# Optimization experiments

Hardware: AMD Instinct MI355X
Metric: run time of the kernel (lower is better)

## Reference

```python
import jax, jax.numpy as jnp
import numpy as np

B, S, NH, D_IN = 64, 512, 4, 256   # batch, seq_len, rnn n_head, input_dim
H = 256                            # hidden_dim == attention activation_dim
AH = 256                           # attention_hidden_dim (attn out_dim)
OUT = 3                            # output_dim (sentiment classes)


def setup_inputs() -> dict:
    key = jax.random.key(0)
    ks = jax.random.split(key, 9)
    def p(k, shape, scale=0.05):
        return jax.random.normal(k, shape, dtype=jnp.float32) * scale
    return dict(
        x=jax.random.normal(ks[0], (B, S, NH, D_IN), dtype=jnp.float32),
        Wk=p(ks[1], (D_IN, H)), bk=jnp.zeros((H,), jnp.float32),
        Wq=p(ks[2], (H, H)),    bq=jnp.zeros((H,), jnp.float32),
        w_mlp=p(ks[3], (2 * H,)),
        Wproj=p(ks[4], (H, AH)), bproj=jnp.zeros((AH,), jnp.float32),
        W1=p(ks[5], (D_IN + AH, H)), b1=jnp.zeros((H,), jnp.float32),
        W2=p(ks[6], (H, H)),    b2=jnp.zeros((H,), jnp.float32),
        Wo=p(ks[7], (NH * H, OUT)), bo=jnp.zeros((OUT,), jnp.float32),
    )


def _cell(x_t, hidden, params):
    Wk, bk, Wq, bq, w_mlp, Wproj, bproj, W1, b1, W2, b2, Wo, bo = params
    kx = x_t @ Wk + bk           # [B, NH, H]  keys from step input
    qx = hidden @ Wq + bq        # [B, NH, H]  queries from hidden state
    w1, w2 = w_mlp[:H], w_mlp[H:]
    # MLP score: s[b,i,j] = tanh(cat(kx[b,j], qx[b,i]) . w) = tanh(kx[b,j].w1 + qx[b,i].w2)
    score = jnp.tanh((qx @ w2)[:, :, None] + (kx @ w1)[:, None, :])  # [B, NH, NH]
    score = jax.nn.softmax(score, axis=-1)
    attn = jnp.einsum('bij,bjh->bih', score, kx) @ Wproj + bproj     # [B, NH, AH]
    concat = jnp.concatenate([x_t, attn], axis=-1)                   # [B, NH, D_IN+AH]
    hidden_new = jax.nn.relu(concat @ W1 + b1) @ W2 + b2             # [B, NH, H]
    logits = hidden_new.reshape(B, NH * H) @ Wo + bo                 # [B, OUT]
    out = jax.nn.log_softmax(logits, axis=-1)
    return out, hidden_new


def reference(x, Wk, bk, Wq, bq, w_mlp, Wproj, bproj, W1, b1, W2, b2, Wo, bo):
    params = (Wk, bk, Wq, bq, w_mlp, Wproj, bproj, W1, b1, W2, b2, Wo, bo)
    h0 = jnp.zeros((B, NH, H), x.dtype)
    xs = jnp.swapaxes(x, 0, 1)  # [S, B, NH, D_IN] for scan over time
    def step(h, x_t):
        out, h_new = _cell(x_t, h, params)
        return h_new, out
    h_final, outs = jax.lax.scan(step, h0, xs)
    # return_sequence=False: last-step log-softmax output and final hidden
    return outs[-1], h_final
```

## Files before the change

### kernel.cpp

```cpp
#include <hip/hip_runtime.h>
#include <hip/hip_bf16.h>
#include <math.h>

#define BB   64
#define SS   512
#define NHH  4
#define DD   256
#define HH   256
#define LDH  264

typedef __attribute__((ext_vector_type(8))) short  short8;
typedef __attribute__((ext_vector_type(4))) float  floatx4;

#define OFF_V2     0
#define OFF_CB1    256
#define OFF_C2     512
#define OFF_CKW    513
#define OFF_QW     768
#define OFF_WK1    1024
#define OFF_BKP    1280
#define OFF_VT     1536
#define OFF_RU     1792
#define OFF_WFUSE  67328
#define OFF_WKF    132864
#define OFF_PACK   198400
#define OFF_CH     263936

__device__ __forceinline__ unsigned short f2b(float f) {
  __hip_bfloat16 h = __float2bfloat16(f);
  return __builtin_bit_cast(unsigned short, h);
}
__device__ __forceinline__ float b2f(unsigned short u) {
  unsigned v = (unsigned)u << 16;
  return __builtin_bit_cast(float, v);
}

__global__ __launch_bounds__(256) void initA_kernel(
    const float* __restrict__ Wproj, const float* __restrict__ W1,
    const float* __restrict__ bk, const float* __restrict__ bproj,
    const float* __restrict__ Wq, const float* __restrict__ w_mlp,
    float* __restrict__ ws)
{
  int tid = threadIdx.x;
  int bx = blockIdx.x;
  const float* W1b = W1 + 256 * 256;
  if (bx < 256) {
    __shared__ float row[256];
    row[tid] = Wproj[bx * 256 + tid];
    __syncthreads();
    float acc = 0.f;
#pragma unroll 8
    for (int k = 0; k < 256; ++k)
      acc = fmaf(row[k], W1b[k * 256 + tid], acc);
    ws[OFF_WFUSE + bx * 256 + tid] = acc;
  } else if (bx == 256) {
    float acc = bproj[tid];
#pragma unroll 8
    for (int k = 0; k < 256; ++k)
      acc = fmaf(bk[k], Wproj[k * 256 + tid], acc);
    ws[OFF_BKP + tid] = acc;
  } else {
    const float4* Wq4 = (const float4*)(Wq + tid * 256);
    const float4* w24 = (const float4*)(w_mlp + 256);
    float a = 0.f;
    for (int k = 0; k < 64; ++k) {
      float4 wv = Wq4[k], xv = w24[k];
      a = fmaf(wv.x, xv.x, fmaf(wv.y, xv.y, fmaf(wv.z, xv.z, fmaf(wv.w, xv.w, a))));
    }
    ws[OFF_VT + tid] = a;
  }
}

__global__ __launch_bounds__(256) void initB_kernel(
    const float* __restrict__ Wk, const float* __restrict__ W1,
    const float* __restrict__ b1, const float* __restrict__ W2,
    const float* __restrict__ b2, const float* __restrict__ bq,
    const float* __restrict__ bk, const float* __restrict__ w_mlp,
    float* __restrict__ ws)
{
  int tid = threadIdx.x;
  int bx = blockIdx.x;
  if (bx < 256) {
    __shared__ float row[256];
    row[tid] = Wk[bx * 256 + tid];
    __syncthreads();
    float acc = 0.f;
    const float* Wf = ws + OFF_WFUSE;
#pragma unroll 8
    for (int k = 0; k < 256; ++k)
      acc = fmaf(row[k], Wf[k * 256 + tid], acc);
    ws[OFF_WKF + bx * 256 + tid] = acc;
  } else if (bx == 256) {
    const float* W1b = W1 + 256 * 256;
    float acc = b1[tid];
#pragma unroll 8
    for (int k = 0; k < 256; ++k)
      acc = fmaf(ws[OFF_BKP + k], W1b[k * 256 + tid], acc);
    ws[OFF_CB1 + tid] = acc;
  } else if (bx == 257) {
    __shared__ float red[256];
    {
      const float4* W24 = (const float4*)(W2 + tid * 256);
      const float4* v4  = (const float4*)(ws + OFF_VT);
      float a = 0.f;
      for (int k = 0; k < 64; ++k) {
        float4 wv = W24[k], xv = v4[k];
        a = fmaf(wv.x, xv.x, fmaf(wv.y, xv.y, fmaf(wv.z, xv.z, fmaf(wv.w, xv.w, a))));
      }
      ws[OFF_V2 + tid] = a;
    }
    red[tid] = bq[tid] * w_mlp[256 + tid];
    __syncthreads();
    for (int s = 128; s; s >>= 1) { if (tid < s) red[tid] += red[tid + s]; __syncthreads(); }
    float s2 = red[0];
    __syncthreads();
    ws[OFF_QW + tid] = s2;
    red[tid] = b2[tid] * ws[OFF_VT + tid];
    __syncthreads();
    for (int s = 128; s; s >>= 1) { if (tid < s) red[tid] += red[tid + s]; __syncthreads(); }
    if (tid == 0) ws[OFF_C2] = red[0] + s2;
    __syncthreads();
    red[tid] = bk[tid] * w_mlp[tid];
    __syncthreads();
    for (int s = 128; s; s >>= 1) { if (tid < s) red[tid] += red[tid + s]; __syncthreads(); }
    if (tid == 0) ws[OFF_CKW] = red[0];
  } else {
    const float4* Wk4 = (const float4*)(Wk + tid * 256);
    const float4* w14 = (const float4*)(w_mlp);
    float a = 0.f;
    for (int k = 0; k < 64; ++k) {
      float4 wv = Wk4[k], xv = w14[k];
      a = fmaf(wv.x, xv.x, fmaf(wv.y, xv.y, fmaf(wv.z, xv.z, fmaf(wv.w, xv.w, a))));
    }
    ws[OFF_WK1 + tid] = a;
  }
}

__global__ __launch_bounds__(256) void initC_kernel(
    const float* __restrict__ W1, float* __restrict__ ws)
{
  int idx = blockIdx.x * 256 + threadIdx.x;
  int mat = idx >> 16;
  int rem = idx & 65535;
  int j    = rem & 7;
  int lane = (rem >> 3) & 63;
  int ks   = (rem >> 9) & 7;
  int pan  = rem >> 12;
  int k = ks * 32 + ((lane >> 4) << 3) + j;
  int n = pan * 16 + (lane & 15);
  float v = (mat == 0) ? ws[OFF_WKF + k * 256 + n] : W1[k * 256 + n];
  ((unsigned short*)(ws + OFF_PACK))[idx] = f2b(v);
}

__device__ __forceinline__ void mfma_gemm4(
    const unsigned short* A_lds, const short8* __restrict__ Bp,
    const float* __restrict__ bias, floatx4 acc[4][4], int l, int w)
{
  int col = l & 15, quad = l >> 4;
#pragma unroll
  for (int pp = 0; pp < 4; ++pp) {
    float bv = bias ? bias[(w * 4 + pp) * 16 + col] : 0.f;
#pragma unroll
    for (int mf = 0; mf < 4; ++mf)
      acc[mf][pp] = (floatx4){bv, bv, bv, bv};
  }
  const short8* Bb = Bp + (size_t)(w * 4) * 512 + l;
  short8 bb[3][4];
#pragma unroll
  for (int pp = 0; pp < 4; ++pp) bb[0][pp] = Bb[pp * 512];
#pragma unroll
  for (int pp = 0; pp < 4; ++pp) bb[1][pp] = Bb[pp * 512 + 64];
#pragma unroll
  for (int kb = 0; kb < 8; ++kb) {
    if (kb + 2 < 8) {
#pragma unroll
      for (int pp = 0; pp < 4; ++pp)
        bb[(kb + 2) % 3][pp] = Bb[pp * 512 + (kb + 2) * 64];
    }
    short8 aa[4];
#pragma unroll
    for (int mf = 0; mf < 4; ++mf)
      aa[mf] = *(const short8*)(A_lds + (mf * 16 + col) * LDH + kb * 32 + quad * 8);
#pragma unroll
    for (int mf = 0; mf < 4; ++mf)
#pragma unroll
      for (int pp = 0; pp < 4; ++pp)
        acc[mf][pp] = __builtin_amdgcn_mfma_f32_16x16x32_bf16(
            aa[mf], bb[kb % 3][pp], acc[mf][pp], 0, 0, 0);
  }
}

__device__ __forceinline__ void acc_to_global(
    unsigned short* __restrict__ dst, const floatx4 acc[4][4],
    int l, int w, int b, int tt)
{
  int col = l & 15, quad = l >> 4;
#pragma unroll
  for (int mf = 0; mf < 4; ++mf)
#pragma unroll
    for (int r = 0; r < 4; ++r) {
      int m2 = mf * 16 + quad * 4 + r;
      size_t base = (((size_t)(tt * 16 + (m2 >> 2)) * 64 + b) * 4 + (m2 & 3)) * 256;
#pragma unroll
      for (int pp = 0; pp < 4; ++pp)
        dst[base + (w * 4 + pp) * 16 + col] = f2b(acc[mf][pp][r]);
    }
}

__global__ __launch_bounds__(256, 3) void pre_kernel(
    const float* __restrict__ x, const float* __restrict__ ws,
    float* __restrict__ kw_c, unsigned short* __restrict__ xw1_c,
    unsigned short* __restrict__ kpw_c, int t0)
{
  __shared__ float kwbuf[256];
  __shared__ __align__(16) unsigned short XS[64 * LDH];

  int b  = blockIdx.x & 63;
  int tt = blockIdx.x >> 6;
  int tid = threadIdx.x;
  int l = tid & 63, w = tid >> 6;

  const float4* xsrc = (const float4*)(x + (size_t)(b * SS + t0 + tt * 16) * NHH * DD);
#pragma unroll
  for (int i = 0; i < 16; ++i) {
    int f4 = i * 256 + tid;
    int r = f4 >> 6, c4 = f4 & 63;
    float4 v = xsrc[f4];
    ushort4 h;
    h.x = f2b(v.x); h.y = f2b(v.y); h.z = f2b(v.z); h.w = f2b(v.w);
    *(ushort4*)&XS[r * LDH + c4 * 4] = h;
  }
  __syncthreads();

  const short8* wp0 = (const short8*)((const unsigned short*)(ws + OFF_PACK));
  const short8* wp1 = (const short8*)((const unsigned short*)(ws + OFF_PACK) + 65536);

  {
    float part = 0.f;
    const unsigned short* trow = XS + l * LDH + w * 64;
#pragma unroll
    for (int j8 = 0; j8 < 8; ++j8) {
      short8 tv = *(const short8*)(trow + j8 * 8);
#pragma unroll
      for (int j = 0; j < 8; ++j)
        part = fmaf(b2f((unsigned short)tv[j]), ws[OFF_WK1 + w * 64 + j8 * 8 + j], part);
    }
    kwbuf[l * 4 + w] = part;
  }

  floatx4 acc[4][4];

  mfma_gemm4(XS, wp0, nullptr, acc, l, w);
  acc_to_global(kpw_c, acc, l, w, b, tt);
  __syncthreads();
  if (tid < 64) {
    float s = kwbuf[tid * 4] + kwbuf[tid * 4 + 1] + kwbuf[tid * 4 + 2] + kwbuf[tid * 4 + 3]
            + ws[OFF_CKW];
    kw_c[((size_t)(tt * 16 + (tid >> 2)) * 64 + b) * 4 + (tid & 3)] = s;
  }

  mfma_gemm4(XS, wp1, ws + OFF_CB1, acc, l, w);
  acc_to_global(xw1_c, acc, l, w, b, tt);
}

__device__ __forceinline__ float wave_reduce_sum(float x) {
#define DPPSTEP(ctrl, rmask)                                                   \
  {                                                                            \
    int _s = __builtin_amdgcn_update_dpp(0, __builtin_bit_cast(int, x),        \
                                         (ctrl), (rmask), 0xf, true);          \
    x += __builtin_bit_cast(float, _s);                                        \
  }
  DPPSTEP(0x111, 0xf)
  DPPSTEP(0x112, 0xf)
  DPPSTEP(0x114, 0xf)
  DPPSTEP(0x118, 0xf)
  DPPSTEP(0x142, 0xa)
  DPPSTEP(0x143, 0xc)
#undef DPPSTEP
  return __builtin_bit_cast(float, __builtin_amdgcn_readlane(__builtin_bit_cast(int, x), 63));
}

__device__ __forceinline__ float tanh_fast(float y) {
  float ex = __expf(2.f * y);
  return 1.f - 2.f * __builtin_amdgcn_rcpf(ex + 1.f);
}

__global__ void seq_kernel(
    const unsigned short* __restrict__ xw1_c, const unsigned short* __restrict__ kpw_c,
    const float* __restrict__ kw_c, float* __restrict__ ws,
    float* __restrict__ relu_u, int t0, int n)
{
  int b = blockIdx.x;
  int tid = threadIdx.x;
  int i = tid >> 6, l = tid & 63;

  float4 v2v = ((const float4*)(ws + OFF_V2))[l];
  float c2 = ws[OFF_C2];
  float qw = ws[OFF_QW + b * 4 + i];

  const ushort4* xw = (const ushort4*)xw1_c;
  const ushort4* kp = (const ushort4*)kpw_c;

  struct Slot { ushort4 x, k0, k1, k2, k3; float4 kw; };

  auto load = [&](Slot& s, int tc) {
    size_t rb_ = (size_t)(tc * 64 + b) * 4;
    s.x  = xw[(rb_ + i) * 64 + l];
    s.k0 = kp[(rb_ + 0) * 64 + l];
    s.k1 = kp[(rb_ + 1) * 64 + l];
    s.k2 = kp[(rb_ + 2) * 64 + l];
    s.k3 = kp[(rb_ + 3) * 64 + l];
    s.kw = *(const float4*)&kw_c[rb_];
  };

  auto step = [&](Slot& s, int t) {
    float e0 = tanh_fast(qw + s.kw.x);
    float e1 = tanh_fast(qw + s.kw.y);
    float e2 = tanh_fast(qw + s.kw.z);
    float e3 = tanh_fast(qw + s.kw.w);
    float q0 = __expf(e0), q1 = __expf(e1), q2 = __expf(e2), q3 = __expf(e3);
    float inv = __builtin_amdgcn_rcpf(q0 + q1 + q2 + q3);
    float4 K0 = {b2f(s.k0.x), b2f(s.k0.y), b2f(s.k0.z), b2f(s.k0.w)};
    float4 K1 = {b2f(s.k1.x), b2f(s.k1.y), b2f(s.k1.z), b2f(s.k1.w)};
    float4 K2 = {b2f(s.k2.x), b2f(s.k2.y), b2f(s.k2.z), b2f(s.k2.w)};
    float4 K3 = {b2f(s.k3.x), b2f(s.k3.y), b2f(s.k3.z), b2f(s.k3.w)};
    float4 X  = {b2f(s.x.x), b2f(s.x.y), b2f(s.x.z), b2f(s.x.w)};
    float4 a;
    a.x = fmaf(q0, K0.x, fmaf(q1, K1.x, fmaf(q2, K2.x, q3 * K3.x)));
    a.y = fmaf(q0, K0.y, fmaf(q1, K1.y, fmaf(q2, K2.y, q3 * K3.y)));
    a.z = fmaf(q0, K0.z, fmaf(q1, K1.z, fmaf(q2, K2.z, q3 * K3.z)));
    a.w = fmaf(q0, K0.w, fmaf(q1, K1.w, fmaf(q2, K2.w, q3 * K3.w)));
    float4 u;
    u.x = fmaf(a.x, inv, X.x); u.y = fmaf(a.y, inv, X.y);
    u.z = fmaf(a.z, inv, X.z); u.w = fmaf(a.w, inv, X.w);
    float4 r;
    r.x = fmaxf(u.x, 0.f); r.y = fmaxf(u.y, 0.f);
    r.z = fmaxf(u.z, 0.f); r.w = fmaxf(u.w, 0.f);
    float d = fmaf(r.x, v2v.x, fmaf(r.y, v2v.y, fmaf(r.z, v2v.z, r.w * v2v.w)));
    qw = wave_reduce_sum(d) + c2;
    if (t0 + t == SS - 1)
      *(float4*)&relu_u[(size_t)(b * 4 + i) * 256 + l * 4] = r;
  };

  Slot s[8];
#pragma unroll
  for (int j = 0; j < 8; ++j) load(s[j], j < n ? j : n - 1);

  for (int t = 0; t < n; t += 8) {
#pragma unroll
    for (int j = 0; j < 8; ++j) {
      step(s[j], t + j);
      int nt = t + 8 + j;
      load(s[j], nt < n ? nt : n - 1);
    }
  }
  if (l == 0) ws[OFF_QW + b * 4 + i] = qw;
}

__global__ __launch_bounds__(256) void final_hidden_kernel(
    const float* __restrict__ relu_u, const float* __restrict__ W2,
    const float* __restrict__ b2, float* __restrict__ out)
{
  __shared__ float rs[256];
  int row = blockIdx.x;
  int tid = threadIdx.x;
  rs[tid] = relu_u[(size_t)row * 256 + tid];
  __syncthreads();
  float acc = b2[tid];
  for (int k = 0; k < 256; ++k) acc = fmaf(rs[k], W2[k * 256 + tid], acc);
  out[192 + (size_t)row * 256 + tid] = acc;
}

__global__ __launch_bounds__(256) void final_logits_kernel(
    const float* __restrict__ hf, const float* __restrict__ Wo,
    const float* __restrict__ bo, float* __restrict__ outp)
{
  __shared__ float r0[256], r1[256], r2[256];
  int b = blockIdx.x;
  int tid = threadIdx.x;
  float a0 = 0.f, a1 = 0.f, a2 = 0.f;
  for (int k = tid; k < 1024; k += 256) {
    float h = hf[(size_t)b * 1024 + k];
    a0 = fmaf(h, Wo[k * 3 + 0], a0);
    a1 = fmaf(h, Wo[k * 3 + 1], a1);
    a2 = fmaf(h, Wo[k * 3 + 2], a2);
  }
  r0[tid] = a0; r1[tid] = a1; r2[tid] = a2;
  __syncthreads();
  for (int s = 128; s; s >>= 1) {
    if (tid < s) { r0[tid] += r0[tid + s]; r1[tid] += r1[tid + s]; r2[tid] += r2[tid + s]; }
    __syncthreads();
  }
  if (tid == 0) {
    float l0 = r0[0] + bo[0], l1 = r1[0] + bo[1], l2 = r2[0] + bo[2];
    float m = fmaxf(l0, fmaxf(l1, l2));
    float lse = m + logf(expf(l0 - m) + expf(l1 - m) + expf(l2 - m));
    outp[b * 3 + 0] = l0 - lse;
    outp[b * 3 + 1] = l1 - lse;
    outp[b * 3 + 2] = l2 - lse;
  }
}

extern "C" void kernel_launch(void* const* d_in, const int* in_sizes, int n_in,
                              void* d_out, int out_size, void* d_ws, size_t ws_size,
                              hipStream_t stream)
{
  const float* x     = (const float*)d_in[0];
  const float* Wk    = (const float*)d_in[1];
  const float* bk    = (const float*)d_in[2];
  const float* Wq    = (const float*)d_in[3];
  const float* bq    = (const float*)d_in[4];
  const float* w_mlp = (const float*)d_in[5];
  const float* Wproj = (const float*)d_in[6];
  const float* bproj = (const float*)d_in[7];
  const float* W1    = (const float*)d_in[8];
  const float* b1    = (const float*)d_in[9];
  const float* W2    = (const float*)d_in[10];
  const float* b2    = (const float*)d_in[11];
  const float* Wo    = (const float*)d_in[12];
  const float* bo    = (const float*)d_in[13];
  float* out = (float*)d_out;
  float* ws  = (float*)d_ws;

  float* ru = ws + OFF_RU;
  const long per_t = 256 + 65536;

  long ws_floats = (long)(ws_size / 4);
  long avail = ws_floats - (long)OFF_CH;

  int Tc = SS;
  while (Tc > 16 && (long)Tc * per_t > avail) Tc -= 16;

  float* kw_c = ws + OFF_CH;
  unsigned short* xw1_c = (unsigned short*)(kw_c + (size_t)Tc * 256);
  unsigned short* kpw_c = xw1_c + (size_t)Tc * 65536;

  initA_kernel<<<258, 256, 0, stream>>>(Wproj, W1, bk, bproj, Wq, w_mlp, ws);
  initB_kernel<<<259, 256, 0, stream>>>(Wk, W1, b1, W2, b2, bq, bk, w_mlp, ws);
  initC_kernel<<<512, 256, 0, stream>>>(W1, ws);

  for (int t0 = 0; t0 < SS; t0 += Tc) {
    int n = (SS - t0) < Tc ? (SS - t0) : Tc;
    pre_kernel<<<64 * (n / 16), 256, 0, stream>>>(x, ws, kw_c, xw1_c, kpw_c, t0);
    seq_kernel<<<64, 256, 0, stream>>>(xw1_c, kpw_c, kw_c, ws, ru, t0, n);
  }

  final_hidden_kernel<<<BB * NHH, 256, 0, stream>>>(ru, W2, b2, out);
  final_logits_kernel<<<BB, 256, 0, stream>>>(out + 192, Wo, bo, out);
}
```

Before: 463.0 us.

## Stage pre_kernel outputs through LDS and add prefetch waves to seq_kernel

pre_kernel now computes both MFMA GEMMs before writing, stages each bf16 result tile in shared memory and stores it to global memory with coalesced 16-byte writes instead of scattered 2-byte stores. It also drops occupancy to 2 blocks per SIMD. seq_kernel is split into one block per (batch, head), 256 blocks in total. Wave 0 runs the recurrence, and three helper waves load upcoming timesteps' data ahead of time so it is warm in cache, synchronised by per-group barriers. The cost is extra barriers in the serial loop and redundant global reads.

Measured after the change: 466.3 us. Within noise of the previous version (+0.7%).

```diff
diff --git a/kernel.cpp b/kernel.cpp
--- a/kernel.cpp
+++ b/kernel.cpp
@@ -190,24 +190,34 @@
   }
 }
 
-__device__ __forceinline__ void acc_to_global(
-    unsigned short* __restrict__ dst, const floatx4 acc[4][4],
-    int l, int w, int b, int tt)
+__device__ __forceinline__ void acc_to_lds(
+    unsigned short* D, const floatx4 acc[4][4], int l, int w)
 {
   int col = l & 15, quad = l >> 4;
 #pragma unroll
   for (int mf = 0; mf < 4; ++mf)
 #pragma unroll
-    for (int r = 0; r < 4; ++r) {
-      int m2 = mf * 16 + quad * 4 + r;
-      size_t base = (((size_t)(tt * 16 + (m2 >> 2)) * 64 + b) * 4 + (m2 & 3)) * 256;
-#pragma unroll
-      for (int pp = 0; pp < 4; ++pp)
-        dst[base + (w * 4 + pp) * 16 + col] = f2b(acc[mf][pp][r]);
-    }
-}
-
-__global__ __launch_bounds__(256, 3) void pre_kernel(
+    for (int pp = 0; pp < 4; ++pp)
+#pragma unroll
+      for (int r = 0; r < 4; ++r)
+        D[(mf * 16 + quad * 4 + r) * LDH + (w * 4 + pp) * 16 + col] = f2b(acc[mf][pp][r]);
+}
+
+__device__ __forceinline__ void lds_to_global_bf16(
+    const unsigned short* S, unsigned short* __restrict__ g, int b, int tt, int tid)
+{
+#pragma unroll
+  for (int it = 0; it < 8; ++it) {
+    int u8 = it * 256 + tid;
+    int r = u8 >> 5;
+    int c8 = u8 & 31;
+    int t = tt * 16 + (r >> 2), head = r & 3;
+    float4 v = *(const float4*)&S[r * LDH + c8 * 8];
+    *(float4*)&g[(((size_t)t * 64 + b) * 4 + head) * 256 + c8 * 8] = v;
+  }
+}
+
+__global__ __launch_bounds__(256, 2) void pre_kernel(
     const float* __restrict__ x, const float* __restrict__ ws,
     float* __restrict__ kw_c, unsigned short* __restrict__ xw1_c,
     unsigned short* __restrict__ kpw_c, int t0)
@@ -248,19 +258,24 @@
     kwbuf[l * 4 + w] = part;
   }
 
-  floatx4 acc[4][4];
-
-  mfma_gemm4(XS, wp0, nullptr, acc, l, w);
-  acc_to_global(kpw_c, acc, l, w, b, tt);
-  __syncthreads();
+  floatx4 acc1[4][4], acc2[4][4];
+  mfma_gemm4(XS, wp0, nullptr, acc1, l, w);
+  mfma_gemm4(XS, wp1, ws + OFF_CB1, acc2, l, w);
+  __syncthreads();
+
   if (tid < 64) {
     float s = kwbuf[tid * 4] + kwbuf[tid * 4 + 1] + kwbuf[tid * 4 + 2] + kwbuf[tid * 4 + 3]
             + ws[OFF_CKW];
     kw_c[((size_t)(tt * 16 + (tid >> 2)) * 64 + b) * 4 + (tid & 3)] = s;
   }
 
-  mfma_gemm4(XS, wp1, ws + OFF_CB1, acc, l, w);
-  acc_to_global(xw1_c, acc, l, w, b, tt);
+  acc_to_lds(XS, acc1, l, w);
+  __syncthreads();
+  lds_to_global_bf16(XS, kpw_c, b, tt, tid);
+  __syncthreads();
+  acc_to_lds(XS, acc2, l, w);
+  __syncthreads();
+  lds_to_global_bf16(XS, xw1_c, b, tt, tid);
 }
 
 __device__ __forceinline__ float wave_reduce_sum(float x) {
@@ -285,76 +300,111 @@
   return 1.f - 2.f * __builtin_amdgcn_rcpf(ex + 1.f);
 }
 
-__global__ void seq_kernel(
+__global__ __launch_bounds__(256, 1) void seq_kernel(
     const unsigned short* __restrict__ xw1_c, const unsigned short* __restrict__ kpw_c,
     const float* __restrict__ kw_c, float* __restrict__ ws,
     float* __restrict__ relu_u, int t0, int n)
 {
-  int b = blockIdx.x;
+  int b = blockIdx.x & 63;
+  int i = blockIdx.x >> 6;
   int tid = threadIdx.x;
-  int i = tid >> 6, l = tid & 63;
-
-  float4 v2v = ((const float4*)(ws + OFF_V2))[l];
-  float c2 = ws[OFF_C2];
-  float qw = ws[OFF_QW + b * 4 + i];
-
-  const ushort4* xw = (const ushort4*)xw1_c;
-  const ushort4* kp = (const ushort4*)kpw_c;
-
-  struct Slot { ushort4 x, k0, k1, k2, k3; float4 kw; };
-
-  auto load = [&](Slot& s, int tc) {
-    size_t rb_ = (size_t)(tc * 64 + b) * 4;
-    s.x  = xw[(rb_ + i) * 64 + l];
-    s.k0 = kp[(rb_ + 0) * 64 + l];
-    s.k1 = kp[(rb_ + 1) * 64 + l];
-    s.k2 = kp[(rb_ + 2) * 64 + l];
-    s.k3 = kp[(rb_ + 3) * 64 + l];
-    s.kw = *(const float4*)&kw_c[rb_];
-  };
-
-  auto step = [&](Slot& s, int t) {
-    float e0 = tanh_fast(qw + s.kw.x);
-    float e1 = tanh_fast(qw + s.kw.y);
-    float e2 = tanh_fast(qw + s.kw.z);
-    float e3 = tanh_fast(qw + s.kw.w);
-    float q0 = __expf(e0), q1 = __expf(e1), q2 = __expf(e2), q3 = __expf(e3);
-    float inv = __builtin_amdgcn_rcpf(q0 + q1 + q2 + q3);
-    float4 K0 = {b2f(s.k0.x), b2f(s.k0.y), b2f(s.k0.z), b2f(s.k0.w)};
-    float4 K1 = {b2f(s.k1.x), b2f(s.k1.y), b2f(s.k1.z), b2f(s.k1.w)};
-    float4 K2 = {b2f(s.k2.x), b2f(s.k2.y), b2f(s.k2.z), b2f(s.k2.w)};
-    float4 K3 = {b2f(s.k3.x), b2f(s.k3.y), b2f(s.k3.z), b2f(s.k3.w)};
-    float4 X  = {b2f(s.x.x), b2f(s.x.y), b2f(s.x.z), b2f(s.x.w)};
-    float4 a;
-    a.x = fmaf(q0, K0.x, fmaf(q1, K1.x, fmaf(q2, K2.x, q3 * K3.x)));
-    a.y = fmaf(q0, K0.y, fmaf(q1, K1.y, fmaf(q2, K2.y, q3 * K3.y)));
-    a.z = fmaf(q0, K0.z, fmaf(q1, K1.z, fmaf(q2, K2.z, q3 * K3.z)));
-    a.w = fmaf(q0, K0.w, fmaf(q1, K1.w, fmaf(q2, K2.w, q3 * K3.w)));
-    float4 u;
-    u.x = fmaf(a.x, inv, X.x); u.y = fmaf(a.y, inv, X.y);
-    u.z = fmaf(a.z, inv, X.z); u.w = fmaf(a.w, inv, X.w);
-    float4 r;
-    r.x = fmaxf(u.x, 0.f); r.y = fmaxf(u.y, 0.f);
-    r.z = fmaxf(u.z, 0.f); r.w = fmaxf(u.w, 0.f);
-    float d = fmaf(r.x, v2v.x, fmaf(r.y, v2v.y, fmaf(r.z, v2v.z, r.w * v2v.w)));
-    qw = wave_reduce_sum(d) + c2;
-    if (t0 + t == SS - 1)
-      *(float4*)&relu_u[(size_t)(b * 4 + i) * 256 + l * 4] = r;
-  };
-
-  Slot s[8];
-#pragma unroll
-  for (int j = 0; j < 8; ++j) load(s[j], j < n ? j : n - 1);
-
-  for (int t = 0; t < n; t += 8) {
-#pragma unroll
-    for (int j = 0; j < 8; ++j) {
-      step(s[j], t + j);
-      int nt = t + 8 + j;
-      load(s[j], nt < n ? nt : n - 1);
-    }
-  }
-  if (l == 0) ws[OFF_QW + b * 4 + i] = qw;
+  int wv = tid >> 6, l = tid & 63;
+  int ngroups = n >> 3;
+
+  if (wv == 0) {
+    float4 v2v = ((const float4*)(ws + OFF_V2))[l];
+    float c2 = ws[OFF_C2];
+    float qw = ws[OFF_QW + b * 4 + i];
+
+    const ushort4* xw = (const ushort4*)xw1_c;
+    const ushort4* kp = (const ushort4*)kpw_c;
+
+    struct Slot { ushort4 x, k0, k1, k2, k3; float4 kw; };
+
+    auto load = [&](Slot& s, int tc) {
+      size_t rb_ = (size_t)(tc * 64 + b) * 4;
+      s.x  = xw[(rb_ + i) * 64 + l];
+      s.k0 = kp[(rb_ + 0) * 64 + l];
+      s.k1 = kp[(rb_ + 1) * 64 + l];
+      s.k2 = kp[(rb_ + 2) * 64 + l];
+      s.k3 = kp[(rb_ + 3) * 64 + l];
+      s.kw = *(const float4*)&kw_c[rb_];
+    };
+
+    auto step = [&](Slot& s, int t) {
+      float e0 = tanh_fast(qw + s.kw.x);
+      float e1 = tanh_fast(qw + s.kw.y);
+      float e2 = tanh_fast(qw + s.kw.z);
+      float e3 = tanh_fast(qw + s.kw.w);
+      float q0 = __expf(e0), q1 = __expf(e1), q2 = __expf(e2), q3 = __expf(e3);
+      float inv = __builtin_amdgcn_rcpf(q0 + q1 + q2 + q3);
+      float4 K0 = {b2f(s.k0.x), b2f(s.k0.y), b2f(s.k0.z), b2f(s.k0.w)};
+      float4 K1 = {b2f(s.k1.x), b2f(s.k1.y), b2f(s.k1.z), b2f(s.k1.w)};
+      float4 K2 = {b2f(s.k2.x), b2f(s.k2.y), b2f(s.k2.z), b2f(s.k2.w)};
+      float4 K3 = {b2f(s.k3.x), b2f(s.k3.y), b2f(s.k3.z), b2f(s.k3.w)};
+      float4 X  = {b2f(s.x.x), b2f(s.x.y), b2f(s.x.z), b2f(s.x.w)};
+      float4 a;
+      a.x = fmaf(q0, K0.x, fmaf(q1, K1.x, fmaf(q2, K2.x, q3 * K3.x)));
+      a.y = fmaf(q0, K0.y, fmaf(q1, K1.y, fmaf(q2, K2.y, q3 * K3.y)));
+      a.z = fmaf(q0, K0.z, fmaf(q1, K1.z, fmaf(q2, K2.z, q3 * K3.z)));
+      a.w = fmaf(q0, K0.w, fmaf(q1, K1.w, fmaf(q2, K2.w, q3 * K3.w)));
+      float4 u;
+      u.x = fmaf(a.x, inv, X.x); u.y = fmaf(a.y, inv, X.y);
+      u.z = fmaf(a.z, inv, X.z); u.w = fmaf(a.w, inv, X.w);
+      float4 r;
+      r.x = fmaxf(u.x, 0.f); r.y = fmaxf(u.y, 0.f);
+      r.z = fmaxf(u.z, 0.f); r.w = fmaxf(u.w, 0.f);
+      float d = fmaf(r.x, v2v.x, fmaf(r.y, v2v.y, fmaf(r.z, v2v.z, r.w * v2v.w)));
+      qw = wave_reduce_sum(d) + c2;
+      if (t0 + t == SS - 1)
+        *(float4*)&relu_u[(size_t)(b * 4 + i) * 256 + l * 4] = r;
+    };
+
+    Slot s[8];
+#pragma unroll
+    for (int j = 0; j < 8; ++j) load(s[j], j < n ? j : n - 1);
+
+    for (int g = 0; g < ngroups; ++g) {
+      int t = g * 8;
+#pragma unroll
+      for (int j = 0; j < 8; ++j) {
+        step(s[j], t + j);
+        int nt = t + 8 + j;
+        load(s[j], nt < n ? nt : n - 1);
+      }
+      __builtin_amdgcn_s_barrier();
+    }
+    if (l == 0) ws[OFF_QW + b * 4 + i] = qw;
+  } else {
+    float4 f4[9];
+    float4 sacc = {0.f, 0.f, 0.f, 0.f};
+#pragma unroll
+    for (int q = 0; q < 9; ++q) f4[q] = (float4){0.f, 0.f, 0.f, 0.f};
+
+    for (int g = 0; g < ngroups; ++g) {
+#pragma unroll
+      for (int q = 0; q < 9; ++q) {
+        sacc.x += f4[q].x; sacc.y += f4[q].y;
+        sacc.z += f4[q].z; sacc.w += f4[q].w;
+      }
+      int tbase = g * 8 + 16;
+#pragma unroll
+      for (int tl = 0; tl < 3; ++tl) {
+        int tloc = (wv - 1) + 3 * tl; if (tloc > 7) tloc = 7;
+        int t = tbase + tloc; if (t > n - 1) t = n - 1;
+        size_t rb_ = (size_t)(t * 64 + b) * 4;
+        const float4* kpb = (const float4*)(kpw_c + rb_ * 256);
+        f4[tl * 3 + 0] = kpb[l];
+        f4[tl * 3 + 1] = kpb[64 + l];
+        const float4* xwb = (const float4*)(xw1_c + (rb_ + i) * 256);
+        const float4* kwb = (const float4*)(kw_c + rb_);
+        f4[tl * 3 + 2] = (l < 32) ? xwb[l] : kwb[0];
+      }
+      __builtin_amdgcn_s_barrier();
+    }
+    float z = sacc.x + sacc.y + sacc.z + sacc.w;
+    asm volatile("" :: "v"(z));
+  }
 }
 
 __global__ __launch_bounds__(256) void final_hidden_kernel(
@@ -442,7 +492,7 @@
   for (int t0 = 0; t0 < SS; t0 += Tc) {
     int n = (SS - t0) < Tc ? (SS - t0) : Tc;
     pre_kernel<<<64 * (n / 16), 256, 0, stream>>>(x, ws, kw_c, xw1_c, kpw_c, t0);
-    seq_kernel<<<64, 256, 0, stream>>>(xw1_c, kpw_c, kw_c, ws, ru, t0, n);
+    seq_kernel<<<256, 256, 0, stream>>>(xw1_c, kpw_c, kw_c, ws, ru, t0, n);
   }
 
   final_hidden_kernel<<<BB * NHH, 256, 0, stream>>>(ru, W2, b2, out);
```
